# Performance work log

Measured on AMD Instinct MI355X. Metric: run time of the kernel, lower is better.

The kernel has to match this reference:

```python
import jax, jax.numpy as jnp
import numpy as np


def _gru_dir(x, kernel, rec_kernel, bias):
    """Keras GRU (reset_after=True). x: [B,T,D] -> [B,T,U]."""
    B, T, D = x.shape
    U = rec_kernel.shape[0]
    # Precompute input projections for all timesteps: [B,T,3U]
    xw = jnp.einsum('btd,dk->btk', x, kernel) + bias[0]
    h0 = jnp.zeros((B, U), dtype=x.dtype)

    def step(h, xw_t):
        rec = h @ rec_kernel + bias[1]            # [B,3U]
        xz, xr, xh = jnp.split(xw_t, 3, axis=-1)
        rz, rr, rh = jnp.split(rec, 3, axis=-1)
        z = jax.nn.sigmoid(xz + rz)
        r = jax.nn.sigmoid(xr + rr)
        hh = jnp.tanh(xh + r * rh)
        h_new = z * h + (1.0 - z) * hh
        return h_new, h_new

    _, hs = jax.lax.scan(step, h0, jnp.swapaxes(xw, 0, 1))  # hs: [T,B,U]
    return jnp.swapaxes(hs, 0, 1)


def setup_inputs() -> dict:
    key = jax.random.key(0)
    ks = jax.random.split(key, 7)
    B, T, D, U = 64, 1024, 256, 256
    s_in = 1.0 / np.sqrt(D)
    s_rec = 1.0 / np.sqrt(U)
    return {
        'x': jax.random.normal(ks[0], (B, T, D), jnp.float32),
        'kernel_f': jax.random.normal(ks[1], (D, 3 * U), jnp.float32) * s_in,
        'rec_kernel_f': jax.random.normal(ks[2], (U, 3 * U), jnp.float32) * s_rec,
        'bias_f': jnp.zeros((2, 3 * U), jnp.float32),
        'kernel_b': jax.random.normal(ks[3], (D, 3 * U), jnp.float32) * s_in,
        'rec_kernel_b': jax.random.normal(ks[4], (U, 3 * U), jnp.float32) * s_rec,
        'bias_b': jnp.zeros((2, 3 * U), jnp.float32),
    }


def reference(x, kernel_f, rec_kernel_f, bias_f, kernel_b, rec_kernel_b, bias_b):
    # Forward direction
    out_f = _gru_dir(x, kernel_f, rec_kernel_f, bias_f)
    # Backward direction: reverse time, run GRU, reverse output back
    xb = x[:, ::-1, :]
    out_b = _gru_dir(xb, kernel_b, rec_kernel_b, bias_b)[:, ::-1, :]
    # Bidirectional merge_mode='concat'
    return jnp.concatenate([out_f, out_b], axis=-1)  # [B,T,2U]
```

## Files before the change

kernel.cpp:

```cpp
#include <hip/hip_runtime.h>
#include <hip/hip_fp16.h>
#include <hip/hip_bf16.h>

typedef __attribute__((ext_vector_type(8))) short bf16x8;
typedef __attribute__((ext_vector_type(4))) float f32x4;

__device__ __forceinline__ short f2bf(float f) {
    unsigned u = __builtin_bit_cast(unsigned, f);
    unsigned r = (u + 0x7FFFu + ((u >> 16) & 1u)) >> 16;
    return (short)r;
}
__device__ __forceinline__ float fast_rcp(float x) {
    return __builtin_amdgcn_rcpf(x);
}
__device__ __forceinline__ float fast_exp(float x) {
    return __builtin_amdgcn_exp2f(x * 1.4426950408889634f);
}

__global__ __launch_bounds__(256) void prep_kernel(
    const float* __restrict__ kf, const float* __restrict__ kb,
    const float* __restrict__ rf, const float* __restrict__ rb,
    short* __restrict__ kT, short* __restrict__ rTf, short* __restrict__ rTb)
{
    int idx = blockIdx.x * 256 + threadIdx.x;
    int n = idx >> 8;
    int k = idx & 255;
    const float* src = (n < 768) ? kf : kb;
    int nn = (n < 768) ? n : (n - 768);
    kT[idx] = f2bf(src[k * 768 + nn]);
    if (n < 768) {
        rTf[idx] = f2bf(rf[k * 768 + n]);
        rTb[idx] = f2bf(rb[k * 768 + n]);
    }
}

__global__ __launch_bounds__(256) void proj_kernel(
    const float* __restrict__ x, const short* __restrict__ kT,
    const float* __restrict__ bias_f, const float* __restrict__ bias_b,
    char* __restrict__ xwp_f, char* __restrict__ xwp_b)
{
    __shared__ short lA[64][264];
    __shared__ short lB[128][264];

    const int tid = threadIdx.x;
    const int m0 = blockIdx.x * 64;
    const int n0 = blockIdx.y * 128;

    const int b_blk  = m0 >> 10;
    const int bg     = b_blk >> 4;
    const int rowg   = b_blk & 15;
    const int hi_t   = rowg >> 2;
    const int i_t    = rowg & 3;
    const int tbase  = m0 & 1023;

#pragma unroll
    for (int rep = 0; rep < 16; ++rep) {
        int lin = rep * 256 + tid;
        int r = lin >> 6;
        int c4 = lin & 63;
        float4 v = *(const float4*)(x + (size_t)(m0 + r) * 256 + c4 * 4);
        short4 s;
        s.x = f2bf(v.x); s.y = f2bf(v.y); s.z = f2bf(v.z); s.w = f2bf(v.w);
        *(short4*)&lA[r][c4 * 4] = s;
    }
#pragma unroll
    for (int rep = 0; rep < 16; ++rep) {
        int lin = rep * 256 + tid;
        int r = lin >> 5;
        int c8 = lin & 31;
        uint4 v = *(const uint4*)(kT + (size_t)(n0 + r) * 256 + c8 * 8);
        *(uint4*)&lB[r][c8 * 8] = v;
    }
    __syncthreads();

    const int w = tid >> 6, l = tid & 63;
    const int l15 = l & 15, hi = l >> 4;

    bf16x8 a[8];
#pragma unroll
    for (int kt = 0; kt < 8; ++kt)
        a[kt] = *(const bf16x8*)&lA[w * 16 + l15][kt * 32 + hi * 8];

#pragma unroll
    for (int j = 0; j < 8; ++j) {
        f32x4 acc = {0.f, 0.f, 0.f, 0.f};
#pragma unroll
        for (int kt = 0; kt < 8; ++kt) {
            bf16x8 b = *(const bf16x8*)&lB[j * 16 + l15][kt * 32 + hi * 8];
            acc = __builtin_amdgcn_mfma_f32_16x16x32_bf16(a[kt], b, acc, 0, 0, 0);
        }
        int ng = n0 + j * 16 + l15;
        int dirb = ng >= 768;
        int nn = ng - (dirb ? 768 : 0);
        const float* bias = dirb ? bias_b : bias_f;
        float badd = bias[nn] + ((nn < 512) ? bias[768 + nn] : 0.f);
        char* basep = dirb ? xwp_b : xwp_f;

        int g   = nn >> 8;
        int cg2 = nn & 255;
        int wt  = cg2 >> 4;
        int lane_t = hi_t * 16 + (cg2 & 15);

#pragma unroll
        for (int i = 0; i < 4; ++i) {
            int t = tbase + w * 16 + hi * 4 + i;
            unsigned short hv = __builtin_bit_cast(unsigned short,
                                    __float2half(acc[i] + badd));
            if (g < 2) {
                *(unsigned short*)(basep + ((size_t)bg << 24) + ((size_t)t << 14)
                                   + (wt << 10) + (lane_t << 4) + ((g * 4 + i_t) << 1)) = hv;
            } else {
                *(unsigned short*)(basep + 67108864u + ((size_t)bg << 23) + ((size_t)t << 13)
                                   + (wt << 9) + (lane_t << 3) + (i_t << 1)) = hv;
            }
        }
    }
}

#define GRU_STEP(PR, PW)                                                     \
  {                                                                          \
    uint4  xv16 = *(const uint4*)xp16;  xp16 += step16;                      \
    uint2  xv8  = *(const uint2*)xp8;   xp8  += step8;                       \
    unsigned bbase = 0;                                                      \
    asm volatile("" : "+v"(bbase));    \
    f32x4 az = {0.f,0.f,0.f,0.f}, ar = {0.f,0.f,0.f,0.f},                    \
          ah = {0.f,0.f,0.f,0.f};                                            \
    _Pragma("unroll") for (int kt = 0; kt < 8; ++kt) {                       \
      bf16x8 aq = *(const bf16x8*)((const char*)hfrag + (PR)*8192            \
                                   + kt * 1024 + l * 16);                    \
      az = __builtin_amdgcn_mfma_f32_16x16x32_bf16(aq, Bz[kt], az, 0,0,0);   \
      ar = __builtin_amdgcn_mfma_f32_16x16x32_bf16(aq, Br[kt], ar, 0,0,0);   \
      bf16x8 bh;                                                             \
      if (kt < 3) bh = Bh[kt];                                               \
      else bh = *(const bf16x8*)((const char*)bfrag + bbase                  \
                                 + (kt - 3) * 16384 + w * 1024 + l * 16);    \
      ah = __builtin_amdgcn_mfma_f32_16x16x32_bf16(aq, bh, ah, 0,0,0);       \
    }                                                                        \
    const __half* hx = (const __half*)&xv16;                                 \
    const __half* hh8 = (const __half*)&xv8;                                 \
    _Pragma("unroll") for (int i = 0; i < 4; ++i) {                          \
      float xz = __half2float(hx[i]);                                        \
      float xr = __half2float(hx[4 + i]);                                    \
      float xh = __half2float(hh8[i]);                                       \
      float zi  = fast_rcp(1.f + fast_exp(-(xz + az[i])));                   \
      float rri = fast_rcp(1.f + fast_exp(-(xr + ar[i])));                   \
      float pre = xh + rri * (ah[i] + b1h);                                  \
      pre = fminf(fmaxf(pre, -15.f), 15.f);                                  \
      float e = fast_exp(2.f * pre);                                         \
      float hhv = (e - 1.f) * fast_rcp(e + 1.f);                             \
      float hn = hhv + zi * (hold[i] - hhv);                                 \
      hold[i] = hn;                                                          \
      opbase[i * 524288] = hn;                                               \
      *(short*)((char*)hfrag + (PW)*8192 + wb + i * 16) = f2bf(hn);          \
    }                                                                        \
    opbase += ostep;                                                         \
    asm volatile("s_waitcnt lgkmcnt(0)\n\ts_barrier" ::: "memory");          \
  }

__global__ __launch_bounds__(1024) void gru_kernel(
    const char* __restrict__ xwp_f, const char* __restrict__ xwp_b,
    const short* __restrict__ recT_f, const short* __restrict__ recT_b,
    const float* __restrict__ bias_f, const float* __restrict__ bias_b,
    float* __restrict__ out)
{
    __shared__ short hfrag[2][8][64][8];
    __shared__ short bfrag[5][16][64][8];

    const int tid = threadIdx.x;
    const int w = tid >> 6, l = tid & 63;
    const int l15 = l & 15, hi = l >> 4;
    const int dir = blockIdx.x >> 2;
    const int bg  = blockIdx.x & 3;
    const int b0  = bg * 16;

    const char*  xwp  = dir ? xwp_b  : xwp_f;
    const short* recT = dir ? recT_b : recT_f;
    const float* bias = dir ? bias_b : bias_f;

    const int cg = w * 16 + l15;
    const float b1h = bias[768 + 512 + cg];

    ((int4*)hfrag)[tid] = make_int4(0, 0, 0, 0);

    const char* recTc = (const char*)recT;
    unsigned offz = (((unsigned)(cg)       * 256u) + hi * 8u) * 2u;
    unsigned offr = (((unsigned)(256 + cg) * 256u) + hi * 8u) * 2u;
    unsigned offh = (((unsigned)(512 + cg) * 256u) + hi * 8u) * 2u;
    bf16x8 Bz[8], Br[8], Bh[3];
#pragma unroll
    for (int kt = 0; kt < 8; ++kt) {
        Bz[kt] = *(const bf16x8*)(recTc + offz + kt * 64);
        Br[kt] = *(const bf16x8*)(recTc + offr + kt * 64);
    }
#pragma unroll
    for (int kt = 0; kt < 3; ++kt)
        Bh[kt] = *(const bf16x8*)(recTc + offh + kt * 64);
#pragma unroll
    for (int kt = 3; kt < 8; ++kt) {
        bf16x8 tmp = *(const bf16x8*)(recTc + offh + kt * 64);
        *(bf16x8*)((char*)bfrag + (kt - 3) * 16384 + w * 1024 + l * 16) = tmp;
    }

    const int t0 = dir ? 1023 : 0;
    const long step16 = dir ? -16384 : 16384;
    const long step8  = dir ? -8192  : 8192;
    const char* xp16 = xwp + ((size_t)bg << 24) + ((size_t)t0 << 14)
                       + (w << 10) + (l << 4);
    const char* xp8  = xwp + 67108864u + ((size_t)bg << 23) + ((size_t)t0 << 13)
                       + (w << 9) + (l << 3);

    const long ostep = dir ? -512 : 512;
    float* opbase = out + (size_t)(b0 + hi * 4) * 524288 + (size_t)t0 * 512
                    + (size_t)dir * 256 + cg;

    const unsigned wb = (unsigned)(cg >> 5) * 1024u
                      + ((((unsigned)cg >> 3) & 3u) * 16u) * 16u
                      + (unsigned)(hi * 4) * 16u + ((unsigned)(l15 & 7)) * 2u;

    f32x4 hold = {0.f, 0.f, 0.f, 0.f};
    __syncthreads();

    for (int su = 0; su < 512; ++su) {
        GRU_STEP(0, 1)
        GRU_STEP(1, 0)
    }
}

extern "C" void kernel_launch(void* const* d_in, const int* in_sizes, int n_in,
                              void* d_out, int out_size, void* d_ws, size_t ws_size,
                              hipStream_t stream) {
    const float* x   = (const float*)d_in[0];
    const float* kf  = (const float*)d_in[1];
    const float* rf  = (const float*)d_in[2];
    const float* bf_ = (const float*)d_in[3];
    const float* kb  = (const float*)d_in[4];
    const float* rb  = (const float*)d_in[5];
    const float* bb_ = (const float*)d_in[6];

    char* ws = (char*)d_ws;
    char* xwp_f = ws;
    char* xwp_b = ws + 100663296;
    short* rTf  = (short*)(ws + 201326592);
    short* rTb  = (short*)(ws + 201719808);
    short* kT   = (short*)(ws + 202113024);
    float* out  = (float*)d_out;

    hipLaunchKernelGGL(prep_kernel, dim3(1536), dim3(256), 0, stream,
                       kf, kb, rf, rb, kT, rTf, rTb);
    hipLaunchKernelGGL(proj_kernel, dim3(1024, 12), dim3(256), 0, stream,
                       x, kT, bf_, bb_, xwp_f, xwp_b);
    hipLaunchKernelGGL(gru_kernel, dim3(8), dim3(1024), 0, stream,
                       xwp_f, xwp_b, rTf, rTb, bf_, bb_, out);
}
```

Before: 2.033 ms.

## Prefetch next-step xw, keep all recurrent weights in registers, fold bias into MFMA init

Double-buffers the per-timestep input projection loads so the next step's xw is fetched one step ahead, hiding global latency on the serial recurrence. All eight h-gate weight fragments now stay in registers instead of five being read from LDS each step, which removes the bfrag LDS traffic. The accumulators are seeded with the x projections and the bias, tanh is computed through a sigmoid form without clamping, and the bf16 packing uses v_cvt_pk_bf16_f32. Holding more weights in registers raises VGPR pressure at 1024 threads per block and could cause spills, and dropping the clamp relies on the sigmoid form staying finite.

```diff
diff --git a/kernel.cpp b/kernel.cpp
--- a/kernel.cpp
+++ b/kernel.cpp
@@ -117,41 +117,46 @@
     }
 }
 
-#define GRU_STEP(PR, PW)                                                     \
+#define GRU_STEP(PR, PW, XC16, XC8, XN16, XN8)                               \
   {                                                                          \
-    uint4  xv16 = *(const uint4*)xp16;  xp16 += step16;                      \
-    uint2  xv8  = *(const uint2*)xp8;   xp8  += step8;                       \
-    unsigned bbase = 0;                                                      \
-    asm volatile("" : "+v"(bbase));    \
-    f32x4 az = {0.f,0.f,0.f,0.f}, ar = {0.f,0.f,0.f,0.f},                    \
-          ah = {0.f,0.f,0.f,0.f};                                            \
+    XN16 = *(const uint4*)xp16;  xp16 += step16;                             \
+    XN8  = *(const uint2*)xp8;   xp8  += step8;                              \
+    const __half* hx  = (const __half*)&XC16;                                \
+    const __half* hx8 = (const __half*)&XC8;                                 \
+    f32x4 az, ar, ah;                                                        \
+    _Pragma("unroll") for (int i = 0; i < 4; ++i) {                          \
+      az[i] = __half2float(hx[i]);                                           \
+      ar[i] = __half2float(hx[4 + i]);                                       \
+      ah[i] = b1h;                                                           \
+    }                                                                        \
     _Pragma("unroll") for (int kt = 0; kt < 8; ++kt) {                       \
       bf16x8 aq = *(const bf16x8*)((const char*)hfrag + (PR)*8192            \
                                    + kt * 1024 + l * 16);                    \
       az = __builtin_amdgcn_mfma_f32_16x16x32_bf16(aq, Bz[kt], az, 0,0,0);   \
       ar = __builtin_amdgcn_mfma_f32_16x16x32_bf16(aq, Br[kt], ar, 0,0,0);   \
-      bf16x8 bh;                                                             \
-      if (kt < 3) bh = Bh[kt];                                               \
-      else bh = *(const bf16x8*)((const char*)bfrag + bbase                  \
-                                 + (kt - 3) * 16384 + w * 1024 + l * 16);    \
-      ah = __builtin_amdgcn_mfma_f32_16x16x32_bf16(aq, bh, ah, 0,0,0);       \
-    }                                                                        \
-    const __half* hx = (const __half*)&xv16;                                 \
-    const __half* hh8 = (const __half*)&xv8;                                 \
+      ah = __builtin_amdgcn_mfma_f32_16x16x32_bf16(aq, Bh[kt], ah, 0,0,0);   \
+    }                                                                        \
+    float hn[4];                                                             \
     _Pragma("unroll") for (int i = 0; i < 4; ++i) {                          \
-      float xz = __half2float(hx[i]);                                        \
-      float xr = __half2float(hx[4 + i]);                                    \
-      float xh = __half2float(hh8[i]);                                       \
-      float zi  = fast_rcp(1.f + fast_exp(-(xz + az[i])));                   \
-      float rri = fast_rcp(1.f + fast_exp(-(xr + ar[i])));                   \
-      float pre = xh + rri * (ah[i] + b1h);                                  \
-      pre = fminf(fmaxf(pre, -15.f), 15.f);                                  \
-      float e = fast_exp(2.f * pre);                                         \
-      float hhv = (e - 1.f) * fast_rcp(e + 1.f);                             \
-      float hn = hhv + zi * (hold[i] - hhv);                                 \
-      hold[i] = hn;                                                          \
-      opbase[i * 524288] = hn;                                               \
-      *(short*)((char*)hfrag + (PW)*8192 + wb + i * 16) = f2bf(hn);          \
+      float zi  = fast_rcp(1.f + fast_exp(-az[i]));                          \
+      float rri = fast_rcp(1.f + fast_exp(-ar[i]));                          \
+      float xh  = __half2float(hx8[i]);                                      \
+      float pre = xh + rri * ah[i];                                          \
+      float sg  = fast_rcp(1.f + fast_exp(-2.f * pre));                      \
+      float hh  = 2.f * sg - 1.f;                                            \
+      float h2  = hh + zi * (hold[i] - hh);                                  \
+      hold[i] = h2;  hn[i] = h2;                                             \
+      opbase[i * 524288] = h2;                                               \
+    }                                                                        \
+    unsigned pk0, pk1;                                                       \
+    asm("v_cvt_pk_bf16_f32 %0, %1, %2" : "=v"(pk0) : "v"(hn[0]), "v"(hn[1]));\
+    asm("v_cvt_pk_bf16_f32 %0, %1, %2" : "=v"(pk1) : "v"(hn[2]), "v"(hn[3]));\
+    {                                                                        \
+      char* hb = (char*)hfrag + (PW)*8192 + wb;                              \
+      *(short*)(hb)      = (short)(pk0 & 0xffff);                            \
+      *(short*)(hb + 16) = (short)(pk0 >> 16);                               \
+      *(short*)(hb + 32) = (short)(pk1 & 0xffff);                            \
+      *(short*)(hb + 48) = (short)(pk1 >> 16);                               \
     }                                                                        \
     opbase += ostep;                                                         \
     asm volatile("s_waitcnt lgkmcnt(0)\n\ts_barrier" ::: "memory");          \
@@ -164,7 +169,6 @@
     float* __restrict__ out)
 {
     __shared__ short hfrag[2][8][64][8];
-    __shared__ short bfrag[5][16][64][8];
 
     const int tid = threadIdx.x;
     const int w = tid >> 6, l = tid & 63;
@@ -186,19 +190,12 @@
     unsigned offz = (((unsigned)(cg)       * 256u) + hi * 8u) * 2u;
     unsigned offr = (((unsigned)(256 + cg) * 256u) + hi * 8u) * 2u;
     unsigned offh = (((unsigned)(512 + cg) * 256u) + hi * 8u) * 2u;
-    bf16x8 Bz[8], Br[8], Bh[3];
+    bf16x8 Bz[8], Br[8], Bh[8];
 #pragma unroll
     for (int kt = 0; kt < 8; ++kt) {
         Bz[kt] = *(const bf16x8*)(recTc + offz + kt * 64);
         Br[kt] = *(const bf16x8*)(recTc + offr + kt * 64);
-    }
-#pragma unroll
-    for (int kt = 0; kt < 3; ++kt)
         Bh[kt] = *(const bf16x8*)(recTc + offh + kt * 64);
-#pragma unroll
-    for (int kt = 3; kt < 8; ++kt) {
-        bf16x8 tmp = *(const bf16x8*)(recTc + offh + kt * 64);
-        *(bf16x8*)((char*)bfrag + (kt - 3) * 16384 + w * 1024 + l * 16) = tmp;
     }
 
     const int t0 = dir ? 1023 : 0;
@@ -217,12 +214,17 @@
                       + ((((unsigned)cg >> 3) & 3u) * 16u) * 16u
                       + (unsigned)(hi * 4) * 16u + ((unsigned)(l15 & 7)) * 2u;
 
+    uint4 xA16, xB16;
+    uint2 xA8,  xB8;
+    xA16 = *(const uint4*)xp16;  xp16 += step16;
+    xA8  = *(const uint2*)xp8;   xp8  += step8;
+
     f32x4 hold = {0.f, 0.f, 0.f, 0.f};
     __syncthreads();
 
     for (int su = 0; su < 512; ++su) {
-        GRU_STEP(0, 1)
-        GRU_STEP(1, 0)
+        GRU_STEP(0, 1, xA16, xA8, xB16, xB8)
+        GRU_STEP(1, 0, xB16, xB8, xA16, xA8)
     }
 }
 
```

Measured after the change: 3.161 ms. 55.5% more time.

## Hold more recurrent h-gate weights in registers and streamline gate math

Applied to the files above, without the earlier changes.

Keeps five of the eight h-gate weight fragments in VGPRs instead of three, which shrinks the LDS-staged portion, and hoists the LDS fragment load ahead of the z/r MFMAs. The tanh is rewritten as 2*sigmoid(2x)-1 without clamping. The bf16 conversion of the new hidden state now uses the packed v_cvt_pk_bf16_f32 instruction. Together these aim to cut LDS traffic and per-step ALU latency on the serial recurrence, at the cost of 16 more vector registers per thread in a 1024-thread block.

```diff
diff --git a/kernel.cpp b/kernel.cpp
--- a/kernel.cpp
+++ b/kernel.cpp
@@ -128,30 +128,36 @@
     _Pragma("unroll") for (int kt = 0; kt < 8; ++kt) {                       \
       bf16x8 aq = *(const bf16x8*)((const char*)hfrag + (PR)*8192            \
                                    + kt * 1024 + l * 16);                    \
+      bf16x8 bh;                                                             \
+      if (kt < 5) bh = Bh[kt];                                               \
+      else bh = *(const bf16x8*)((const char*)bfrag + bbase                  \
+                                 + (kt - 5) * 16384 + w * 1024 + l * 16);    \
       az = __builtin_amdgcn_mfma_f32_16x16x32_bf16(aq, Bz[kt], az, 0,0,0);   \
       ar = __builtin_amdgcn_mfma_f32_16x16x32_bf16(aq, Br[kt], ar, 0,0,0);   \
-      bf16x8 bh;                                                             \
-      if (kt < 3) bh = Bh[kt];                                               \
-      else bh = *(const bf16x8*)((const char*)bfrag + bbase                  \
-                                 + (kt - 3) * 16384 + w * 1024 + l * 16);    \
       ah = __builtin_amdgcn_mfma_f32_16x16x32_bf16(aq, bh, ah, 0,0,0);       \
     }                                                                        \
-    const __half* hx = (const __half*)&xv16;                                 \
-    const __half* hh8 = (const __half*)&xv8;                                 \
+    const __half* hx  = (const __half*)&xv16;                                \
+    const __half* hx8 = (const __half*)&xv8;                                 \
+    float hn[4];                                                             \
     _Pragma("unroll") for (int i = 0; i < 4; ++i) {                          \
-      float xz = __half2float(hx[i]);                                        \
-      float xr = __half2float(hx[4 + i]);                                    \
-      float xh = __half2float(hh8[i]);                                       \
-      float zi  = fast_rcp(1.f + fast_exp(-(xz + az[i])));                   \
-      float rri = fast_rcp(1.f + fast_exp(-(xr + ar[i])));                   \
-      float pre = xh + rri * (ah[i] + b1h);                                  \
-      pre = fminf(fmaxf(pre, -15.f), 15.f);                                  \
-      float e = fast_exp(2.f * pre);                                         \
-      float hhv = (e - 1.f) * fast_rcp(e + 1.f);                             \
-      float hn = hhv + zi * (hold[i] - hhv);                                 \
-      hold[i] = hn;                                                          \
-      opbase[i * 524288] = hn;                                               \
-      *(short*)((char*)hfrag + (PW)*8192 + wb + i * 16) = f2bf(hn);          \
+      float zi  = fast_rcp(1.f + fast_exp(-(__half2float(hx[i]) + az[i])));  \
+      float rri = fast_rcp(1.f + fast_exp(-(__half2float(hx[4+i]) + ar[i])));\
+      float pre = __half2float(hx8[i]) + rri * (ah[i] + b1h);                \
+      float sg  = fast_rcp(1.f + fast_exp(-2.f * pre));                      \
+      float hh  = 2.f * sg - 1.f;                                            \
+      float h2  = hh + zi * (hold[i] - hh);                                  \
+      hold[i] = h2;  hn[i] = h2;                                             \
+      opbase[i * 524288] = h2;                                               \
+    }                                                                        \
+    unsigned pk0, pk1;                                                       \
+    asm("v_cvt_pk_bf16_f32 %0, %1, %2" : "=v"(pk0) : "v"(hn[0]), "v"(hn[1]));\
+    asm("v_cvt_pk_bf16_f32 %0, %1, %2" : "=v"(pk1) : "v"(hn[2]), "v"(hn[3]));\
+    {                                                                        \
+      char* hb = (char*)hfrag + (PW)*8192 + wb;                              \
+      *(short*)(hb)      = (short)(pk0 & 0xffff);                            \
+      *(short*)(hb + 16) = (short)(pk0 >> 16);                               \
+      *(short*)(hb + 32) = (short)(pk1 & 0xffff);                            \
+      *(short*)(hb + 48) = (short)(pk1 >> 16);                               \
     }                                                                        \
     opbase += ostep;                                                         \
     asm volatile("s_waitcnt lgkmcnt(0)\n\ts_barrier" ::: "memory");          \
@@ -164,7 +170,7 @@
     float* __restrict__ out)
 {
     __shared__ short hfrag[2][8][64][8];
-    __shared__ short bfrag[5][16][64][8];
+    __shared__ short bfrag[3][16][64][8];
 
     const int tid = threadIdx.x;
     const int w = tid >> 6, l = tid & 63;
@@ -186,19 +192,19 @@
     unsigned offz = (((unsigned)(cg)       * 256u) + hi * 8u) * 2u;
     unsigned offr = (((unsigned)(256 + cg) * 256u) + hi * 8u) * 2u;
     unsigned offh = (((unsigned)(512 + cg) * 256u) + hi * 8u) * 2u;
-    bf16x8 Bz[8], Br[8], Bh[3];
+    bf16x8 Bz[8], Br[8], Bh[5];
 #pragma unroll
     for (int kt = 0; kt < 8; ++kt) {
         Bz[kt] = *(const bf16x8*)(recTc + offz + kt * 64);
         Br[kt] = *(const bf16x8*)(recTc + offr + kt * 64);
     }
 #pragma unroll
-    for (int kt = 0; kt < 3; ++kt)
+    for (int kt = 0; kt < 5; ++kt)
         Bh[kt] = *(const bf16x8*)(recTc + offh + kt * 64);
 #pragma unroll
-    for (int kt = 3; kt < 8; ++kt) {
+    for (int kt = 5; kt < 8; ++kt) {
         bf16x8 tmp = *(const bf16x8*)(recTc + offh + kt * 64);
-        *(bf16x8*)((char*)bfrag + (kt - 3) * 16384 + w * 1024 + l * 16) = tmp;
+        *(bf16x8*)((char*)bfrag + (kt - 5) * 16384 + w * 1024 + l * 16) = tmp;
     }
 
     const int t0 = dir ? 1023 : 0;
```

Result: faster. 1.867 ms (-8.2%).
